# Optimization experiments

Hardware: AMD Instinct MI355X
Metric: run time of the kernel (lower is better)

## Reference

```python
import jax, jax.numpy as jnp
import numpy as np

# Log-signature at depth m=3, d channels, expressed in the full tensor basis
# (iisignature 'expanded' convention; the Lyndon-basis output of method '' is a
# fixed linear projection of these coefficients).

def _chen_step(carry, dx):
    # carry: signature levels S1 [B,d], S2 [B,d,d], S3 [B,d,d,d]
    # dx: increment of one segment, [B,d]. Segment signature E = exp(dx).
    S1, S2, S3 = carry
    E2 = 0.5 * jnp.einsum('bi,bj->bij', dx, dx)
    E3 = (1.0 / 6.0) * jnp.einsum('bi,bj,bk->bijk', dx, dx, dx)
    nS1 = S1 + dx
    nS2 = S2 + jnp.einsum('bi,bj->bij', S1, dx) + E2
    nS3 = (S3
           + jnp.einsum('bij,bk->bijk', S2, dx)
           + jnp.einsum('bi,bjk->bijk', S1, E2)
           + E3)
    return (nS1, nS2, nS3), None


def _logsig(x):
    # x: [B, L, d] path. Returns expanded log-signature [B, d + d^2 + d^3].
    B, L, d = x.shape
    dx = jnp.swapaxes(x[:, 1:] - x[:, :-1], 0, 1)  # [L-1, B, d]
    init = (jnp.zeros((B, d), x.dtype),
            jnp.zeros((B, d, d), x.dtype),
            jnp.zeros((B, d, d, d), x.dtype))
    (S1, S2, S3), _ = jax.lax.scan(_chen_step, init, dx)
    # log(1 + S) truncated at level 3 in the tensor algebra
    l1 = S1
    l2 = S2 - 0.5 * jnp.einsum('bi,bj->bij', S1, S1)
    l3 = (S3
          - 0.5 * (jnp.einsum('bi,bjk->bijk', S1, S2)
                   + jnp.einsum('bij,bk->bijk', S2, S1))
          + (1.0 / 3.0) * jnp.einsum('bi,bj,bk->bijk', S1, S1, S1))
    return jnp.concatenate(
        [l1.reshape(B, -1), l2.reshape(B, -1), l3.reshape(B, -1)], axis=-1)


def setup_inputs() -> dict:
    key = jax.random.key(0)
    B, L, d = 2048, 256, 8
    steps = 0.1 * jax.random.normal(key, (B, L, d), dtype=jnp.float32)
    x = jnp.cumsum(steps, axis=1)  # random-walk paths keep signatures well-scaled
    return {"x": x}


def reference(x):
    return _logsig(x)
```

## Files before the change

### kernel.cpp

```cpp
#include <hip/hip_runtime.h>


#define WPB 4
#define LEN 256
#define DCH 8
#define NSTEPS (LEN - 1)
#define OUTSTRIDE (DCH + DCH*DCH + DCH*DCH*DCH)

__global__ __launch_bounds__(256) void logsig_kernel(const float* __restrict__ x,
                                                     float* __restrict__ out) {
    __shared__ float dxbuf[WPB][2048];
    __shared__ float s1buf[WPB][8];
    __shared__ float s2buf[WPB][64];

    const int tid  = threadIdx.x;
    const int w    = tid >> 6;
    const int lane = tid & 63;
    const int i    = lane >> 3;
    const int j    = lane & 7;
    const int b0   = blockIdx.x * WPB;

    const float4* x4 = (const float4*)x;
    for (int n = tid; n < WPB * 510; n += 256) {
        int wb = n / 510;
        int f  = n - wb * 510;
        const float4* xb = x4 + (size_t)(b0 + wb) * 512;
        float4 a = xb[f];
        float4 c = xb[f + 2];
        float4 dv;
        dv.x = c.x - a.x; dv.y = c.y - a.y; dv.z = c.z - a.z; dv.w = c.w - a.w;
        *((float4*)&dxbuf[wb][f * 4]) = dv;
    }
    __syncthreads();

    float s1 = 0.f, s2 = 0.f;
    float s3[8];
#pragma unroll
    for (int k = 0; k < 8; ++k) s3[k] = 0.f;

    const float* dxw = dxbuf[w];
    const float c6 = 1.f / 6.f;
#pragma unroll 5
    for (int t = 0; t < NSTEPS; ++t) {
        const float* row = dxw + t * 8;
        float4 r0 = *(const float4*)(row);
        float4 r1 = *(const float4*)(row + 4);
        float dxi = row[i];
        float dxj = row[j];

        float tt = fmaf(c6, dxi, 0.5f * s1);
        float w3 = fmaf(tt, dxj, s2);
        s3[0] = fmaf(w3, r0.x, s3[0]);
        s3[1] = fmaf(w3, r0.y, s3[1]);
        s3[2] = fmaf(w3, r0.z, s3[2]);
        s3[3] = fmaf(w3, r0.w, s3[3]);
        s3[4] = fmaf(w3, r1.x, s3[4]);
        s3[5] = fmaf(w3, r1.y, s3[5]);
        s3[6] = fmaf(w3, r1.z, s3[6]);
        s3[7] = fmaf(w3, r1.w, s3[7]);
        float u = fmaf(0.5f, dxi, s1);
        s2 = fmaf(u, dxj, s2);
        s1 += dxi;
    }

    if (j == 0) s1buf[w][i] = s1;
    s2buf[w][lane] = s2;
    __syncthreads();

    float S1r[8], S2rj[8];
#pragma unroll
    for (int k = 0; k < 8; ++k) S1r[k] = s1buf[w][k];
#pragma unroll
    for (int k = 0; k < 8; ++k) S2rj[k] = s2buf[w][j * 8 + k];
    float s1j = s1buf[w][j];

    const int b = b0 + w;
    float* ob = out + (size_t)b * OUTSTRIDE;

    if (lane < 8) ob[lane] = s1buf[w][lane];
    ob[8 + lane] = fmaf(-0.5f * s1, s1j, s2);
    float c3 = (1.f / 3.f) * s1 * s1j;
    float l3[8];
#pragma unroll
    for (int k = 0; k < 8; ++k) {
        l3[k] = s3[k] - 0.5f * (s1 * S2rj[k] + s2 * S1r[k]) + c3 * S1r[k];
    }
    float4 o0 = make_float4(l3[0], l3[1], l3[2], l3[3]);
    float4 o1 = make_float4(l3[4], l3[5], l3[6], l3[7]);
    float* p3 = ob + 72 + lane * 8;
    *(float4*)(p3)     = o0;
    *(float4*)(p3 + 4) = o1;
}

extern "C" void kernel_launch(void* const* d_in, const int* in_sizes, int n_in,
                              void* d_out, int out_size, void* d_ws, size_t ws_size,
                              hipStream_t stream) {
    const float* x = (const float*)d_in[0];
    float* out = (float*)d_out;
    const int B = in_sizes[0] / (LEN * DCH);
    const int blocks = B / WPB;
    hipLaunchKernelGGL(logsig_kernel, dim3(blocks), dim3(256), 0, stream, x, out);
}
```

Baseline: 75.99 us.

## Split increment computation into separate kernel and stream rows via scalar loads

Increments are now computed by a separate kernel into workspace, with the last padded entries zeroed. The scan kernel then reads each wave's shared row through a wave-uniform pointer, so the 8-wide broadcast becomes scalar loads instead of LDS reads. Only the per-lane i/j columns are staged in a transposed LDS buffer, which removes the block-wide barriers. The cost is an extra launch and a round trip of the increments through global memory. The loop now runs 256 steps, relying on the zero padding for the final one.

```diff
diff --git a/kernel.cpp b/kernel.cpp
--- a/kernel.cpp
+++ b/kernel.cpp
@@ -4,12 +4,33 @@
 #define WPB 4
 #define LEN 256
 #define DCH 8
-#define NSTEPS (LEN - 1)
+#define DXSTRIDE 2048
+#define TPAD 260
 #define OUTSTRIDE (DCH + DCH*DCH + DCH*DCH*DCH)
 
-__global__ __launch_bounds__(256) void logsig_kernel(const float* __restrict__ x,
-                                                     float* __restrict__ out) {
-    __shared__ float dxbuf[WPB][2048];
+typedef float floatv8 __attribute__((ext_vector_type(8)));
+
+__global__ __launch_bounds__(256) void compute_dx(const float* __restrict__ x,
+                                                  float* __restrict__ dxg) {
+    const int n = blockIdx.x * 256 + threadIdx.x;
+    const int wb = n >> 9;
+    const int f  = n & 511;
+    const float4* x4 = (const float4*)x;
+    float4* d4 = (float4*)dxg;
+    float4 dv;
+    if (f < 510) {
+        float4 a = x4[(size_t)wb * 512 + f];
+        float4 c = x4[(size_t)wb * 512 + f + 2];
+        dv.x = c.x - a.x; dv.y = c.y - a.y; dv.z = c.z - a.z; dv.w = c.w - a.w;
+    } else {
+        dv.x = 0.f; dv.y = 0.f; dv.z = 0.f; dv.w = 0.f;
+    }
+    d4[(size_t)wb * 512 + f] = dv;
+}
+
+__global__ __launch_bounds__(256) void logsig_scan(const float* __restrict__ dxg,
+                                                   float* __restrict__ out) {
+    __shared__ float dxT[WPB][DCH][TPAD];
     __shared__ float s1buf[WPB][8];
     __shared__ float s2buf[WPB][64];
 
@@ -18,54 +39,57 @@
     const int lane = tid & 63;
     const int i    = lane >> 3;
     const int j    = lane & 7;
-    const int b0   = blockIdx.x * WPB;
+    const int b    = blockIdx.x * WPB + w;
 
-    const float4* x4 = (const float4*)x;
-    for (int n = tid; n < WPB * 510; n += 256) {
-        int wb = n / 510;
-        int f  = n - wb * 510;
-        const float4* xb = x4 + (size_t)(b0 + wb) * 512;
-        float4 a = xb[f];
-        float4 c = xb[f + 2];
-        float4 dv;
-        dv.x = c.x - a.x; dv.y = c.y - a.y; dv.z = c.z - a.z; dv.w = c.w - a.w;
-        *((float4*)&dxbuf[wb][f * 4]) = dv;
+    const int ub = __builtin_amdgcn_readfirstlane(b);
+    const float* __restrict__ rowbase = dxg + (size_t)ub * DXSTRIDE;
+
+    const float4* dx4 = (const float4*)(dxg + (size_t)b * DXSTRIDE);
+    for (int n4 = lane; n4 < 512; n4 += 64) {
+        float4 v = dx4[n4];
+        int c0 = (n4 * 4) & 7;
+        int t  = (n4 * 4) >> 3;
+        dxT[w][c0 + 0][t] = v.x;
+        dxT[w][c0 + 1][t] = v.y;
+        dxT[w][c0 + 2][t] = v.z;
+        dxT[w][c0 + 3][t] = v.w;
     }
-    __syncthreads();
 
     float s1 = 0.f, s2 = 0.f;
     float s3[8];
 #pragma unroll
     for (int k = 0; k < 8; ++k) s3[k] = 0.f;
 
-    const float* dxw = dxbuf[w];
     const float c6 = 1.f / 6.f;
-#pragma unroll 5
-    for (int t = 0; t < NSTEPS; ++t) {
-        const float* row = dxw + t * 8;
-        float4 r0 = *(const float4*)(row);
-        float4 r1 = *(const float4*)(row + 4);
-        float dxi = row[i];
-        float dxj = row[j];
+    const float* vip = &dxT[w][i][0];
+    const float* vjp = &dxT[w][j][0];
 
-        float tt = fmaf(c6, dxi, 0.5f * s1);
-        float w3 = fmaf(tt, dxj, s2);
-        s3[0] = fmaf(w3, r0.x, s3[0]);
-        s3[1] = fmaf(w3, r0.y, s3[1]);
-        s3[2] = fmaf(w3, r0.z, s3[2]);
-        s3[3] = fmaf(w3, r0.w, s3[3]);
-        s3[4] = fmaf(w3, r1.x, s3[4]);
-        s3[5] = fmaf(w3, r1.y, s3[5]);
-        s3[6] = fmaf(w3, r1.z, s3[6]);
-        s3[7] = fmaf(w3, r1.w, s3[7]);
-        float u = fmaf(0.5f, dxi, s1);
-        s2 = fmaf(u, dxj, s2);
-        s1 += dxi;
+    for (int tb = 0; tb < LEN; tb += 4) {
+        float4 vi = *(const float4*)(vip + tb);
+        float4 vj = *(const float4*)(vjp + tb);
+#pragma unroll
+        for (int u = 0; u < 4; ++u) {
+            floatv8 r = *(const floatv8*)(rowbase + ((tb + u) << 3));
+            float dxi = (u == 0) ? vi.x : (u == 1) ? vi.y : (u == 2) ? vi.z : vi.w;
+            float dxj = (u == 0) ? vj.x : (u == 1) ? vj.y : (u == 2) ? vj.z : vj.w;
+            float tt = fmaf(c6, dxi, 0.5f * s1);
+            float w3 = fmaf(tt, dxj, s2);
+            s3[0] = fmaf(w3, r[0], s3[0]);
+            s3[1] = fmaf(w3, r[1], s3[1]);
+            s3[2] = fmaf(w3, r[2], s3[2]);
+            s3[3] = fmaf(w3, r[3], s3[3]);
+            s3[4] = fmaf(w3, r[4], s3[4]);
+            s3[5] = fmaf(w3, r[5], s3[5]);
+            s3[6] = fmaf(w3, r[6], s3[6]);
+            s3[7] = fmaf(w3, r[7], s3[7]);
+            float uu = fmaf(0.5f, dxi, s1);
+            s2 = fmaf(uu, dxj, s2);
+            s1 += dxi;
+        }
     }
 
     if (j == 0) s1buf[w][i] = s1;
     s2buf[w][lane] = s2;
-    __syncthreads();
 
     float S1r[8], S2rj[8];
 #pragma unroll
@@ -74,22 +98,18 @@
     for (int k = 0; k < 8; ++k) S2rj[k] = s2buf[w][j * 8 + k];
     float s1j = s1buf[w][j];
 
-    const int b = b0 + w;
     float* ob = out + (size_t)b * OUTSTRIDE;
-
     if (lane < 8) ob[lane] = s1buf[w][lane];
     ob[8 + lane] = fmaf(-0.5f * s1, s1j, s2);
+
     float c3 = (1.f / 3.f) * s1 * s1j;
     float l3[8];
 #pragma unroll
-    for (int k = 0; k < 8; ++k) {
+    for (int k = 0; k < 8; ++k)
         l3[k] = s3[k] - 0.5f * (s1 * S2rj[k] + s2 * S1r[k]) + c3 * S1r[k];
-    }
-    float4 o0 = make_float4(l3[0], l3[1], l3[2], l3[3]);
-    float4 o1 = make_float4(l3[4], l3[5], l3[6], l3[7]);
     float* p3 = ob + 72 + lane * 8;
-    *(float4*)(p3)     = o0;
-    *(float4*)(p3 + 4) = o1;
+    *(float4*)(p3)     = make_float4(l3[0], l3[1], l3[2], l3[3]);
+    *(float4*)(p3 + 4) = make_float4(l3[4], l3[5], l3[6], l3[7]);
 }
 
 extern "C" void kernel_launch(void* const* d_in, const int* in_sizes, int n_in,
@@ -97,7 +117,8 @@
                               hipStream_t stream) {
     const float* x = (const float*)d_in[0];
     float* out = (float*)d_out;
+    float* dxg = (float*)d_ws;
     const int B = in_sizes[0] / (LEN * DCH);
-    const int blocks = B / WPB;
-    hipLaunchKernelGGL(logsig_kernel, dim3(blocks), dim3(256), 0, stream, x, out);
+    hipLaunchKernelGGL(compute_dx, dim3(B * 2), dim3(256), 0, stream, x, dxg);
+    hipLaunchKernelGGL(logsig_scan, dim3(B / WPB), dim3(256), 0, stream, dxg, out);
 }
```

Result: slower. 82.04 us (+8.0%).

## Split each path's Chen scan across four wavefronts and merge chunk signatures

Applied to the files above, without the earlier changes.

Each block now handles a single batch element instead of four. The 255-step sequential scan is split into four chunks of 64 steps, one per wavefront, with a zero-padded final increment. Chunk signatures are then combined on wave 0 with Chen's identity before the log is taken. This shortens the serial dependency chain per wavefront by about four times. In exchange it adds a shared-memory merge and a barrier, and three of the four waves sit idle during the merge and output stage.

```diff
diff --git a/kernel.cpp b/kernel.cpp
--- a/kernel.cpp
+++ b/kernel.cpp
@@ -1,35 +1,40 @@
 #include <hip/hip_runtime.h>
 
 
-#define WPB 4
 #define LEN 256
 #define DCH 8
-#define NSTEPS (LEN - 1)
+#define NW 4
+#define CHUNK (LEN / NW)
 #define OUTSTRIDE (DCH + DCH*DCH + DCH*DCH*DCH)
 
-__global__ __launch_bounds__(256) void logsig_kernel(const float* __restrict__ x,
-                                                     float* __restrict__ out) {
-    __shared__ float dxbuf[WPB][2048];
-    __shared__ float s1buf[WPB][8];
-    __shared__ float s2buf[WPB][64];
+__global__ __launch_bounds__(256) void logsig_fused(const float* __restrict__ x,
+                                                    float* __restrict__ out) {
+    __shared__ __align__(16) float dxbuf[LEN][DCH];
+    __shared__ __align__(16) float sig1[NW][8];
+    __shared__ __align__(16) float sig2[NW][64];
+    __shared__ __align__(16) float sig3[NW][512];
+    __shared__ __align__(16) float s1buf[8];
+    __shared__ __align__(16) float s2buf[64];
 
     const int tid  = threadIdx.x;
     const int w    = tid >> 6;
     const int lane = tid & 63;
     const int i    = lane >> 3;
     const int j    = lane & 7;
-    const int b0   = blockIdx.x * WPB;
+    const int b    = blockIdx.x;
 
-    const float4* x4 = (const float4*)x;
-    for (int n = tid; n < WPB * 510; n += 256) {
-        int wb = n / 510;
-        int f  = n - wb * 510;
-        const float4* xb = x4 + (size_t)(b0 + wb) * 512;
-        float4 a = xb[f];
-        float4 c = xb[f + 2];
+    const float4* x4 = (const float4*)(x + (size_t)b * (LEN * DCH));
+    float4* d4 = (float4*)&dxbuf[0][0];
+    for (int f = tid; f < 512; f += 256) {
         float4 dv;
-        dv.x = c.x - a.x; dv.y = c.y - a.y; dv.z = c.z - a.z; dv.w = c.w - a.w;
-        *((float4*)&dxbuf[wb][f * 4]) = dv;
+        if (f < 510) {
+            float4 a = x4[f];
+            float4 c = x4[f + 2];
+            dv.x = c.x - a.x; dv.y = c.y - a.y; dv.z = c.z - a.z; dv.w = c.w - a.w;
+        } else {
+            dv.x = 0.f; dv.y = 0.f; dv.z = 0.f; dv.w = 0.f;
+        }
+        d4[f] = dv;
     }
     __syncthreads();
 
@@ -38,58 +43,85 @@
 #pragma unroll
     for (int k = 0; k < 8; ++k) s3[k] = 0.f;
 
-    const float* dxw = dxbuf[w];
     const float c6 = 1.f / 6.f;
-#pragma unroll 5
-    for (int t = 0; t < NSTEPS; ++t) {
-        const float* row = dxw + t * 8;
-        float4 r0 = *(const float4*)(row);
-        float4 r1 = *(const float4*)(row + 4);
-        float dxi = row[i];
-        float dxj = row[j];
-
-        float tt = fmaf(c6, dxi, 0.5f * s1);
-        float w3 = fmaf(tt, dxj, s2);
-        s3[0] = fmaf(w3, r0.x, s3[0]);
-        s3[1] = fmaf(w3, r0.y, s3[1]);
-        s3[2] = fmaf(w3, r0.z, s3[2]);
-        s3[3] = fmaf(w3, r0.w, s3[3]);
-        s3[4] = fmaf(w3, r1.x, s3[4]);
-        s3[5] = fmaf(w3, r1.y, s3[5]);
-        s3[6] = fmaf(w3, r1.z, s3[6]);
-        s3[7] = fmaf(w3, r1.w, s3[7]);
-        float u = fmaf(0.5f, dxi, s1);
-        s2 = fmaf(u, dxj, s2);
-        s1 += dxi;
+    const float* base = &dxbuf[w * CHUNK][0];
+    for (int tb = 0; tb < CHUNK; tb += 4) {
+#pragma unroll
+        for (int u = 0; u < 4; ++u) {
+            const float* row = base + (tb + u) * 8;
+            float4 r0 = *(const float4*)(row);
+            float4 r1 = *(const float4*)(row + 4);
+            float dxi = row[i];
+            float dxj = row[j];
+            float tt = fmaf(c6, dxi, 0.5f * s1);
+            float w3 = fmaf(tt, dxj, s2);
+            s3[0] = fmaf(w3, r0.x, s3[0]);
+            s3[1] = fmaf(w3, r0.y, s3[1]);
+            s3[2] = fmaf(w3, r0.z, s3[2]);
+            s3[3] = fmaf(w3, r0.w, s3[3]);
+            s3[4] = fmaf(w3, r1.x, s3[4]);
+            s3[5] = fmaf(w3, r1.y, s3[5]);
+            s3[6] = fmaf(w3, r1.z, s3[6]);
+            s3[7] = fmaf(w3, r1.w, s3[7]);
+            float uu = fmaf(0.5f, dxi, s1);
+            s2 = fmaf(uu, dxj, s2);
+            s1 += dxi;
+        }
     }
 
-    if (j == 0) s1buf[w][i] = s1;
-    s2buf[w][lane] = s2;
+    if (j == 0) sig1[w][i] = s1;
+    sig2[w][lane] = s2;
+    float* sp = &sig3[w][lane * 8];
+    *(float4*)(sp)     = make_float4(s3[0], s3[1], s3[2], s3[3]);
+    *(float4*)(sp + 4) = make_float4(s3[4], s3[5], s3[6], s3[7]);
     __syncthreads();
+
+    if (w != 0) return;
+
+    for (int c = 1; c < NW; ++c) {
+        float B1i  = sig1[c][i];
+        float B1j  = sig1[c][j];
+        float B2ij = sig2[c][lane];
+        float4 b1a = *(const float4*)&sig1[c][0];
+        float4 b1b = *(const float4*)&sig1[c][4];
+        const float* b2row = &sig2[c][j * 8];
+        float4 b2a = *(const float4*)(b2row);
+        float4 b2b = *(const float4*)(b2row + 4);
+        const float* b3row = &sig3[c][lane * 8];
+        float4 b3a = *(const float4*)(b3row);
+        float4 b3b = *(const float4*)(b3row + 4);
+        float B1k[8]  = {b1a.x, b1a.y, b1a.z, b1a.w, b1b.x, b1b.y, b1b.z, b1b.w};
+        float B2jk[8] = {b2a.x, b2a.y, b2a.z, b2a.w, b2b.x, b2b.y, b2b.z, b2b.w};
+        float B3[8]   = {b3a.x, b3a.y, b3a.z, b3a.w, b3b.x, b3b.y, b3b.z, b3b.w};
+#pragma unroll
+        for (int k = 0; k < 8; ++k)
+            s3[k] = s3[k] + B3[k] + s1 * B2jk[k] + s2 * B1k[k];
+        s2 = s2 + B2ij + s1 * B1j;
+        s1 = s1 + B1i;
+    }
+
+    if (j == 0) s1buf[i] = s1;
+    s2buf[lane] = s2;
 
     float S1r[8], S2rj[8];
 #pragma unroll
-    for (int k = 0; k < 8; ++k) S1r[k] = s1buf[w][k];
+    for (int k = 0; k < 8; ++k) S1r[k] = s1buf[k];
 #pragma unroll
-    for (int k = 0; k < 8; ++k) S2rj[k] = s2buf[w][j * 8 + k];
-    float s1j = s1buf[w][j];
+    for (int k = 0; k < 8; ++k) S2rj[k] = s2buf[j * 8 + k];
+    float s1j = s1buf[j];
 
-    const int b = b0 + w;
     float* ob = out + (size_t)b * OUTSTRIDE;
+    if (lane < 8) ob[lane] = s1buf[lane];
+    ob[8 + lane] = fmaf(-0.5f * s1, s1j, s2);
 
-    if (lane < 8) ob[lane] = s1buf[w][lane];
-    ob[8 + lane] = fmaf(-0.5f * s1, s1j, s2);
     float c3 = (1.f / 3.f) * s1 * s1j;
     float l3[8];
 #pragma unroll
-    for (int k = 0; k < 8; ++k) {
+    for (int k = 0; k < 8; ++k)
         l3[k] = s3[k] - 0.5f * (s1 * S2rj[k] + s2 * S1r[k]) + c3 * S1r[k];
-    }
-    float4 o0 = make_float4(l3[0], l3[1], l3[2], l3[3]);
-    float4 o1 = make_float4(l3[4], l3[5], l3[6], l3[7]);
     float* p3 = ob + 72 + lane * 8;
-    *(float4*)(p3)     = o0;
-    *(float4*)(p3 + 4) = o1;
+    *(float4*)(p3)     = make_float4(l3[0], l3[1], l3[2], l3[3]);
+    *(float4*)(p3 + 4) = make_float4(l3[4], l3[5], l3[6], l3[7]);
 }
 
 extern "C" void kernel_launch(void* const* d_in, const int* in_sizes, int n_in,
@@ -98,6 +130,5 @@
     const float* x = (const float*)d_in[0];
     float* out = (float*)d_out;
     const int B = in_sizes[0] / (LEN * DCH);
-    const int blocks = B / WPB;
-    hipLaunchKernelGGL(logsig_kernel, dim3(blocks), dim3(256), 0, stream, x, out);
+    hipLaunchKernelGGL(logsig_fused, dim3(B), dim3(256), 0, stream, x, out);
 }
```

Measured after the change: 73.22 us. 3.6% less time.
